# Performance work log

Hardware: AMD Instinct MI355X
Metric: run time of the kernel (lower is better)

## Reference

```python
import jax, jax.numpy as jnp
import numpy as np

Q, M, D = 4096, 65536, 1024
TOP_K = 8
EPS = 1e-12  # torch F.normalize eps default


def _l2_normalize(x, axis=-1):
    # matches torch.nn.functional.normalize(p=2): x / max(||x||, eps)
    norm = jnp.sqrt(jnp.sum(x * x, axis=axis, keepdims=True))
    return x / jnp.maximum(norm, EPS)


def setup_inputs() -> dict:
    key = jax.random.key(0)
    kq, kk, kv = jax.random.split(key, 3)
    query_embeddings = jax.random.normal(kq, (Q, D), dtype=jnp.float32)
    keys = jax.random.normal(kk, (M, D), dtype=jnp.float32)
    values = jax.random.normal(kv, (M, D), dtype=jnp.float32)
    return {"query_embeddings": query_embeddings, "keys": keys, "values": values, "top_k": TOP_K}


def reference(query_embeddings, keys, values, top_k):
    # L2-normalize queries and memory keys
    q = _l2_normalize(query_embeddings, axis=1)          # [Q, D]
    k = _l2_normalize(keys, axis=1)                      # [M, D]
    # dense cosine-similarity matmul
    sims = jnp.einsum('qd,md->qm', q, k)                 # [Q, M]
    # top-k selection (sorted descending, like torch.topk)
    topk_vals, topk_idx = jax.lax.top_k(sims, top_k)     # [Q, k]
    # irregular gather of retrieved values
    retrieved = values[topk_idx]                         # [Q, k, D]
    return retrieved
```

## Files before the change

kernel.cpp:

```cpp
#include <hip/hip_runtime.h>
#include <hip/hip_bf16.h>
#include <hip/hip_fp16.h>
#include <math.h>

#define Q_N 4096
#define M_N 65536
#define D_N 1024
#define TOPK 8
#define SEGS 32
#define KPS (M_N / SEGS)
#define CANDS (SEGS * TOPK)
#define NRES 16

#define GBM 256
#define GBN 256
#define GBK32 32
#define GNT32 (D_N / GBK32)
#define CHUNKQ 1024
#define NCHUNK (Q_N / CHUNKQ)
#define NTILES (M_N / GBM)
#define CAP 512

#define BM 128
#define BN 128
#define BK 32
#define NSUB (KPS / BN)
#define NKT (D_N / BK)
#define NSTEP (NSUB * NKT)
#define QT128 (Q_N / BM)

typedef short s16x8 __attribute__((ext_vector_type(8)));
typedef float f32x4 __attribute__((ext_vector_type(4)));

__device__ __forceinline__ bool better(float v0, int i0, float v1, int i1) {
  return (v0 > v1) || (v0 == v1 && i0 < i1);
}

__device__ __forceinline__ unsigned short f2bf(float f) {
  union { __hip_bfloat16 h; unsigned short u; } c;
  c.h = __float2bfloat16(f);
  return c.u;
}
__device__ __forceinline__ unsigned short f2h(float f) {
  union { __half h; unsigned short u; } c;
  c.h = __float2half(f);
  return c.u;
}
__device__ __forceinline__ float h2f(unsigned short u) {
  union { __half h; unsigned short u; } c;
  c.u = u;
  return __half2float(c.h);
}

__device__ __forceinline__ void gll16(void* lds, const void* g) {
  __builtin_amdgcn_global_load_lds(
      (const __attribute__((address_space(1))) unsigned int*)(uintptr_t)g,
      (__attribute__((address_space(3))) unsigned int*)(uintptr_t)lds, 16, 0, 0);
}

__global__ __launch_bounds__(256) void knorm_scale_kernel(const float* __restrict__ keys,
                                                          unsigned short* __restrict__ kb,
                                                          float* __restrict__ rnk) {
  int row = blockIdx.x;
  int tid = threadIdx.x;
  float4 v = reinterpret_cast<const float4*>(keys + (size_t)row * D_N)[tid];
  float s = v.x * v.x + v.y * v.y + v.z * v.z + v.w * v.w;
#pragma unroll
  for (int off = 32; off > 0; off >>= 1) s += __shfl_down(s, off);
  __shared__ float part[4];
  __shared__ float rs;
  int lane = tid & 63, wid = tid >> 6;
  if (lane == 0) part[wid] = s;
  __syncthreads();
  if (tid == 0) {
    float t = part[0] + part[1] + part[2] + part[3];
    rs = 1.0f / fmaxf(sqrtf(t), 1e-12f);
  }
  __syncthreads();
  float r = rs;
  ushort4 o;
  o.x = f2bf(v.x * r); o.y = f2bf(v.y * r); o.z = f2bf(v.z * r); o.w = f2bf(v.w * r);
  reinterpret_cast<ushort4*>(kb + (size_t)row * D_N)[tid] = o;
  if (tid == 0) rnk[row] = r;
}

__global__ __launch_bounds__(256) void qnorm_dual_kernel(const float* __restrict__ q,
                                                         float* __restrict__ qn,
                                                         unsigned short* __restrict__ qb) {
  int row = blockIdx.x;
  int tid = threadIdx.x;
  float4 v = reinterpret_cast<const float4*>(q + (size_t)row * D_N)[tid];
  float s = v.x * v.x + v.y * v.y + v.z * v.z + v.w * v.w;
#pragma unroll
  for (int off = 32; off > 0; off >>= 1) s += __shfl_down(s, off);
  __shared__ float part[4];
  __shared__ float rs;
  int lane = tid & 63, wid = tid >> 6;
  if (lane == 0) part[wid] = s;
  __syncthreads();
  if (tid == 0) {
    float t = part[0] + part[1] + part[2] + part[3];
    rs = 1.0f / fmaxf(sqrtf(t), 1e-12f);
  }
  __syncthreads();
  float r = rs;
  float4 o;
  o.x = v.x * r; o.y = v.y * r; o.z = v.z * r; o.w = v.w * r;
  reinterpret_cast<float4*>(qn + (size_t)row * D_N)[tid] = o;
  ushort4 ob;
  ob.x = f2bf(o.x); ob.y = f2bf(o.y); ob.z = f2bf(o.z); ob.w = f2bf(o.w);
  reinterpret_cast<ushort4*>(qb + (size_t)row * D_N)[tid] = ob;
}

__global__ __launch_bounds__(512, 2) void gemm_kernel(const unsigned short* __restrict__ qb,
                                                      const unsigned short* __restrict__ kb,
                                                      unsigned short* __restrict__ sims,
                                                      float* __restrict__ qmax,
                                                      int qchunk) {
  __shared__ __align__(16) union GSmem {
    struct {
      unsigned short A[3][GBN * GBK32];
      unsigned short B[3][GBM * GBK32];
    } ab;
    unsigned short S[GBN][GBM + 8];
  } smem;

  const int tid = threadIdx.x;
  const int lane = tid & 63;
  const int wid = tid >> 6;
  const int wq = wid & 3;
  const int wk = wid >> 2;

  const int bid = blockIdx.x;
  const int x = bid & 7;
  const int idx = bid >> 3;
  const int keyTile = (x << 5) + (idx >> 2);
  const int qTile = idx & 3;
  const int kbase = keyTile * GBM;
  const int qbase = qchunk * CHUNKQ + qTile * GBN;
  const int qloc0 = qTile * GBN;

  const int srow16 = lane >> 2;
  const int swz32 = (((lane & 3) ^ ((lane >> 2) & 3)) << 3);
  const unsigned short* aRow = qb + (size_t)(qbase + (wid << 5) + srow16) * D_N + swz32;
  const unsigned short* bRow = kb + (size_t)(kbase + (wid << 5) + srow16) * D_N + swz32;

  const int fr = lane & 15;
  const int g = lane >> 4;
  const int cp = ((g ^ (fr & 3)) << 3);

  f32x4 acc[8][4];
#pragma unroll
  for (int m = 0; m < 8; ++m)
#pragma unroll
    for (int n = 0; n < 4; ++n) acc[m][n] = (f32x4)0.0f;

#define STG_A(TT, SL)                                                         \
  {                                                                           \
    unsigned short* d = &smem.ab.A[SL][0] + (wid << 10);                      \
    const unsigned short* s = aRow + ((TT) << 5);                             \
    gll16(d, s);                                                              \
    gll16(d + 512, s + (size_t)16 * D_N);                                     \
  }
#define STG_B(TT, SL)                                                         \
  {                                                                           \
    unsigned short* d = &smem.ab.B[SL][0] + (wid << 10);                      \
    const unsigned short* s = bRow + ((TT) << 5);                             \
    gll16(d, s);                                                              \
    gll16(d + 512, s + (size_t)16 * D_N);                                     \
  }

  STG_A(0, 0) STG_B(0, 0)
  STG_A(1, 1) STG_B(1, 1)

  int slot = 0;
#pragma unroll 1
  for (int t = 0; t < GNT32; ++t) {
    if (t < GNT32 - 1) {
      asm volatile("s_waitcnt vmcnt(4)" ::: "memory");
    } else {
      asm volatile("s_waitcnt vmcnt(0)" ::: "memory");
    }
    __builtin_amdgcn_sched_barrier(0);
    __builtin_amdgcn_s_barrier();
    __builtin_amdgcn_sched_barrier(0);

    const unsigned short* Ac = &smem.ab.A[slot][0];
    const unsigned short* Bc = &smem.ab.B[slot][0];
    int nslot = slot + 2; if (nslot >= 3) nslot -= 3;
    const bool dost = (t + 2) < GNT32;

    s16x8 bq[4], af[4];

#pragma unroll
    for (int mf = 0; mf < 4; ++mf)
      af[mf] = *(const s16x8*)(Bc + ((wk << 7) + (mf << 4) + fr) * GBK32 + cp);
#pragma unroll
    for (int n = 0; n < 4; ++n)
      bq[n] = *(const s16x8*)(Ac + ((wq << 6) + (n << 4) + fr) * GBK32 + cp);
    if (dost) STG_A(t + 2, nslot)
    __builtin_amdgcn_s_barrier();
    __builtin_amdgcn_sched_barrier(0);
    asm volatile("s_waitcnt lgkmcnt(0)" ::: "memory");
    __builtin_amdgcn_sched_barrier(0);
    __builtin_amdgcn_s_setprio(1);
#pragma unroll
    for (int mf = 0; mf < 4; ++mf)
#pragma unroll
      for (int n = 0; n < 4; ++n)
        acc[mf][n] = __builtin_amdgcn_mfma_f32_16x16x32_bf16(af[mf], bq[n], acc[mf][n], 0, 0, 0);
    __builtin_amdgcn_s_setprio(0);
    __builtin_amdgcn_s_barrier();
    __builtin_amdgcn_sched_barrier(0);

#pragma unroll
    for (int mf = 0; mf < 4; ++mf)
      af[mf] = *(const s16x8*)(Bc + ((wk << 7) + 64 + (mf << 4) + fr) * GBK32 + cp);
    if (dost) STG_B(t + 2, nslot)
    __builtin_amdgcn_s_barrier();
    __builtin_amdgcn_sched_barrier(0);
    asm volatile("s_waitcnt lgkmcnt(0)" ::: "memory");
    __builtin_amdgcn_sched_barrier(0);
    __builtin_amdgcn_s_setprio(1);
#pragma unroll
    for (int mf = 0; mf < 4; ++mf)
#pragma unroll
      for (int n = 0; n < 4; ++n)
        acc[4 + mf][n] = __builtin_amdgcn_mfma_f32_16x16x32_bf16(af[mf], bq[n], acc[4 + mf][n], 0, 0, 0);
    __builtin_amdgcn_s_setprio(0);
    __builtin_amdgcn_s_barrier();
    __builtin_amdgcn_sched_barrier(0);

    ++slot; if (slot == 3) slot = 0;
  }
#undef STG_A
#undef STG_B

  __syncthreads();
#pragma unroll
  for (int m = 0; m < 8; ++m)
#pragma unroll
    for (int n = 0; n < 4; ++n)
#pragma unroll
      for (int j = 0; j < 4; ++j)
        smem.S[(wq << 6) + (n << 4) + fr][(wk << 7) + (m << 4) + (g << 2) + j] =
            f2h(acc[m][n][j]);
  __syncthreads();
#pragma unroll 1
  for (int it = 0; it < 16; ++it) {
    int cid = it * 512 + tid;
    int row = cid >> 5;
    int col = (cid & 31) << 3;
    s16x8 vv = *(const s16x8*)&smem.S[row][col];
    *(s16x8*)(sims + (size_t)(qloc0 + row) * M_N + kbase + col) = vv;
  }
  if (tid < 256) {
    float mx = -1e38f;
#pragma unroll 1
    for (int k8 = 0; k8 < 32; ++k8) {
      s16x8 vv = *(const s16x8*)&smem.S[tid][k8 << 3];
#pragma unroll
      for (int e = 0; e < 8; ++e) mx = fmaxf(mx, h2f((unsigned short)vv[e]));
    }
    qmax[(size_t)(qloc0 + tid) * NTILES + keyTile] = mx;
  }
}

__global__ __launch_bounds__(256) void scan2_kernel(const unsigned short* __restrict__ sims,
                                                    const float* __restrict__ qmax,
                                                    int* __restrict__ cand_idx,
                                                    int qchunk) {
  __shared__ float bufv[4][CAP];
  __shared__ int bufi[4][CAP];
  __shared__ int tlist[4][NTILES];
  __shared__ int cnts[4];
  __shared__ int tcnts[4];

  const int tid = threadIdx.x;
  const int lane = tid & 63;
  const int wv = tid >> 6;
  const int q = blockIdx.x * 4 + wv;
  const int qg = qchunk * CHUNKQ + q;
  const unsigned short* row = sims + (size_t)q * M_N;

  if (lane == 0) { cnts[wv] = 0; tcnts[wv] = 0; }
  __syncthreads();

  float4 m4 = *reinterpret_cast<const float4*>(qmax + (size_t)q * NTILES + (lane << 2));
  float tv[4] = {m4.x, m4.y, m4.z, m4.w};
  float keep[4] = {m4.x, m4.y, m4.z, m4.w};
  float T = -1e38f;
#pragma unroll 1
  for (int j = 0; j < 16; ++j) {
    float bv = tv[0]; int bi = (lane << 2);
#pragma unroll
    for (int s = 1; s < 4; ++s)
      if (better(tv[s], (lane << 2) + s, bv, bi)) { bv = tv[s]; bi = (lane << 2) + s; }
#pragma unroll
    for (int off = 32; off > 0; off >>= 1) {
      float ov = __shfl_xor(bv, off);
      int oi = __shfl_xor(bi, off);
      if (better(ov, oi, bv, bi)) { bv = ov; bi = oi; }
    }
    T = bv;
#pragma unroll
    for (int s = 0; s < 4; ++s)
      if ((lane << 2) + s == bi) tv[s] = -1e38f;
  }

#pragma unroll
  for (int s = 0; s < 4; ++s) {
    if (keep[s] >= T) {
      int p = atomicAdd(&tcnts[wv], 1);
      tlist[wv][p] = (lane << 2) + s;
    }
  }
  int tc = tcnts[wv];

#pragma unroll 1
  for (int i = 0; i < tc; ++i) {
    int t = tlist[wv][i];
    ushort4 pk = *reinterpret_cast<const ushort4*>(row + t * GBM + (lane << 2));
    unsigned short pe[4] = {pk.x, pk.y, pk.z, pk.w};
#pragma unroll
    for (int e = 0; e < 4; ++e) {
      float v = h2f(pe[e]);
      if (v >= T) {
        int p = atomicAdd(&cnts[wv], 1);
        if (p < CAP) { bufv[wv][p] = v; bufi[wv][p] = t * GBM + (lane << 2) + e; }
      }
    }
  }
  int n = cnts[wv];
  if (n > CAP) n = CAP;

  float cv[CAP / 64];
  int ci[CAP / 64];
#pragma unroll
  for (int s = 0; s < CAP / 64; ++s) {
    int id = s * 64 + lane;
    bool ok = id < n;
    cv[s] = ok ? bufv[wv][id] : -1e38f;
    ci[s] = ok ? bufi[wv][id] : 0;
  }
#pragma unroll 1
  for (int j = 0; j < 16; ++j) {
    float bv = cv[0]; int bi = ci[0];
#pragma unroll
    for (int s = 1; s < CAP / 64; ++s)
      if (better(cv[s], ci[s], bv, bi)) { bv = cv[s]; bi = ci[s]; }
#pragma unroll
    for (int off = 32; off > 0; off >>= 1) {
      float ov = __shfl_xor(bv, off);
      int oi = __shfl_xor(bi, off);
      if (better(ov, oi, bv, bi)) { bv = ov; bi = oi; }
    }
    if (lane == 0) cand_idx[(size_t)qg * 16 + j] = bi;
#pragma unroll
    for (int s = 0; s < CAP / 64; ++s)
      if (ci[s] == bi) cv[s] = -1e38f;
  }
}

__global__ __launch_bounds__(256) void rescore_kernel(const float* __restrict__ qn,
                                                      const float* __restrict__ keys,
                                                      const float* __restrict__ values,
                                                      const float* __restrict__ rnk,
                                                      const int* __restrict__ cand_idx,
                                                      float* __restrict__ out) {
  const int q = blockIdx.x;
  const int tid = threadIdx.x;
  const int lane = tid & 63;
  const int w = tid >> 6;
  __shared__ int si[16];
  __shared__ float rsc[16];
  if (tid < 16) si[tid] = cand_idx[(size_t)q * 16 + tid];
  __syncthreads();
  const float* qrow = &qn[(size_t)q * D_N + lane * 16];
  float4 qv0 = *reinterpret_cast<const float4*>(qrow + 0);
  float4 qv1 = *reinterpret_cast<const float4*>(qrow + 4);
  float4 qv2 = *reinterpret_cast<const float4*>(qrow + 8);
  float4 qv3 = *reinterpret_cast<const float4*>(qrow + 12);
  for (int c = w; c < 16; c += 4) {
    int id = si[c];
    const float* kr = &keys[(size_t)id * D_N + lane * 16];
    float4 k0 = *reinterpret_cast<const float4*>(kr + 0);
    float4 k1 = *reinterpret_cast<const float4*>(kr + 4);
    float4 k2 = *reinterpret_cast<const float4*>(kr + 8);
    float4 k3 = *reinterpret_cast<const float4*>(kr + 12);
    float s = qv0.x * k0.x + qv0.y * k0.y + qv0.z * k0.z + qv0.w * k0.w
            + qv1.x * k1.x + qv1.y * k1.y + qv1.z * k1.z + qv1.w * k1.w
            + qv2.x * k2.x + qv2.y * k2.y + qv2.z * k2.z + qv2.w * k2.w
            + qv3.x * k3.x + qv3.y * k3.y + qv3.z * k3.z + qv3.w * k3.w;
#pragma unroll
    for (int off = 32; off > 0; off >>= 1) s += __shfl_down(s, off);
    if (lane == 0) rsc[c] = s * rnk[id];
  }
  __syncthreads();
  __shared__ int sel[TOPK];
  if (tid == 0) {
    unsigned used = 0;
    for (int j = 0; j < TOPK; ++j) {
      int best = -1;
      for (int c = 0; c < 16; ++c) {
        if ((used >> c) & 1u) continue;
        if (best < 0 || better(rsc[c], si[c], rsc[best], si[best])) best = c;
      }
      used |= 1u << best;
      sel[j] = si[best];
    }
  }
  __syncthreads();
#pragma unroll
  for (int j = 0; j < TOPK; ++j) {
    int rowi = sel[j];
    float4 v = *reinterpret_cast<const float4*>(&values[(size_t)rowi * D_N + tid * 4]);
    *reinterpret_cast<float4*>(&out[(size_t)q * (TOPK * D_N) + j * D_N + tid * 4]) = v;
  }
}

__global__ __launch_bounds__(256, 3) void simsb_kernel(const unsigned short* __restrict__ qb,
                                                       const unsigned short* __restrict__ kb,
                                                       float* __restrict__ cand_val,
                                                       int* __restrict__ cand_idx) {
  __shared__ __align__(16) union SmemU {
    struct {
      unsigned short A[3][BM * BK];
      unsigned short B[3][BN * BK];
    } ab;
    struct {
      float v[BM * 4 * TOPK];
      int i[BM * 4 * TOPK];
    } mg;
  } smem;

  const int tid = threadIdx.x;
  const int lane = tid & 63;
  const int wid = tid >> 6;

  const int orig = blockIdx.x;
  const int x = orig & 7;
  const int idx = orig >> 3;
  const int qtile = ((x >> 1) << 3) + (idx & 7);
  const int seg = ((x & 1) << 4) + (idx >> 3);
  const int qbase = qtile * BM;
  const int segBase = seg * KPS;

  const int srow = (wid << 5) + (lane >> 2);
  const int scol = (((lane & 3) ^ ((lane >> 3) & 3)) << 3);
  const unsigned short* aSeg = qb + (size_t)(qbase + srow) * D_N + scol;
  const unsigned short* bSeg = kb + (size_t)(segBase + srow) * D_N + scol;

  const int fr = lane & 15;
  const int g = lane >> 4;
  const int chunk_phys = g ^ ((fr >> 1) & 3);
  const unsigned short* rB = &smem.ab.B[0][0] + (fr << 5) + (chunk_phys << 3);
  const unsigned short* rA = &smem.ab.A[0][0] + (((wid << 5) + fr) << 5) + (chunk_phys << 3);

  float lv[2][TOPK];
  int li[2][TOPK];
#pragma unroll
  for (int n = 0; n < 2; ++n)
#pragma unroll
    for (int j = 0; j < TOPK; ++j) { lv[n][j] = -1e30f; li[n][j] = 0x7fffffff; }

  f32x4 acc[8][2];
#pragma unroll
  for (int m = 0; m < 8; ++m)
#pragma unroll
    for (int n = 0; n < 2; ++n) acc[m][n] = (f32x4)0.0f;

#pragma unroll
  for (int p = 0; p < 2; ++p) {
    const unsigned short* aS = aSeg + (p << 5);
    const unsigned short* bS = bSeg + (p << 5);
    unsigned short* Ad = &smem.ab.A[p][0] + (wid << 10);
    unsigned short* Bd = &smem.ab.B[p][0] + (wid << 10);
    gll16(Ad, aS);
    gll16(Ad + 512, aS + (size_t)16 * D_N);
    gll16(Bd, bS);
    gll16(Bd + 512, bS + (size_t)16 * D_N);
  }

  const unsigned short* aP0 = aSeg + 64;
  const unsigned short* aP1 = aP0 + (size_t)16 * D_N;
  const unsigned short* bP0 = bSeg + 64;
  const unsigned short* bP1 = bP0 + (size_t)16 * D_N;

#define SWAIT_(N) asm volatile("s_waitcnt vmcnt(" #N ")" ::: "memory")
#define SWAIT(N) SWAIT_(N)

#define FOLD(V)                                                               \
  {                                                                           \
    const int kb0 = segBase + (((V) >> 5) << 7) + (g << 2);                   \
    _Pragma("unroll")                                                         \
    for (int n = 0; n < 2; ++n)                                               \
      _Pragma("unroll")                                                       \
      for (int m = 0; m < 8; ++m) {                                           \
        float q0 = acc[m][n][0], q1 = acc[m][n][1];                           \
        float q2 = acc[m][n][2], q3 = acc[m][n][3];                           \
        acc[m][n] = (f32x4)0.0f;                                              \
        float mx = fmaxf(fmaxf(q0, q1), fmaxf(q2, q3));                       \
        const int id0 = kb0 + (m << 4);                                       \
        if (better(mx, id0, lv[n][TOPK - 1], li[n][TOPK - 1])) {              \
          float vals[4] = {q0, q1, q2, q3};                                   \
          _Pragma("unroll")                                                   \
          for (int j = 0; j < 4; ++j) {                                       \
            float val = vals[j];                                              \
            int id = id0 + j;                                                 \
            if (better(val, id, lv[n][TOPK - 1], li[n][TOPK - 1])) {          \
              float cv = val; int ci = id;                                    \
              _Pragma("unroll")                                               \
              for (int p = 0; p < TOPK; ++p) {                                \
                if (better(cv, ci, lv[n][p], li[n][p])) {                     \
                  float tv = lv[n][p]; int ti = li[n][p];                     \
                  lv[n][p] = cv; li[n][p] = ci;                               \
                  cv = tv; ci = ti;                                           \
                }                                                             \
              }                                                               \
            }                                                                 \
          }                                                                   \
        }                                                                     \
      }                                                                       \
  }

#define STEP(V, SLOT, WAITN, RESTAGE)                                         \
  {                                                                           \
    SWAIT(WAITN);                                                             \
    __builtin_amdgcn_sched_barrier(0);                                        \
    __builtin_amdgcn_s_barrier();                                             \
    __builtin_amdgcn_sched_barrier(0);                                        \
    if (RESTAGE) {                                                            \
      unsigned short* Ad = &smem.ab.A[((SLOT) + 2) % 3][0] + (wid << 10);     \
      unsigned short* Bd = &smem.ab.B[((SLOT) + 2) % 3][0] + (wid << 10);     \
      gll16(Ad, aP0);                                                         \
      gll16(Ad + 512, aP1);                                                   \
      gll16(Bd, bP0);                                                         \
      gll16(Bd + 512, bP1);                                                   \
    }                                                                         \
    {                                                                         \
      const bool wrp = (((V) & 31) == 29);                                    \
      const int dA = wrp ? -992 : 32;                                         \
      const int dB = wrp ? 130080 : 32;                                       \
      aP0 += dA; aP1 += dA; bP0 += dB; bP1 += dB;                             \
    }                                                                         \
    s16x8 af[8], bq[2];                                                       \
    _Pragma("unroll")                                                         \
    for (int m = 0; m < 8; ++m)                                               \
      af[m] = *(const s16x8*)(rB + (SLOT) * 4096 + (m << 9));                 \
    bq[0] = *(const s16x8*)(rA + (SLOT) * 4096);                              \
    bq[1] = *(const s16x8*)(rA + (SLOT) * 4096 + 512);                        \
    __builtin_amdgcn_s_setprio(1);                                            \
    _Pragma("unroll")                                                         \
    for (int m = 0; m < 8; ++m) {                                             \
      acc[m][0] = __builtin_amdgcn_mfma_f32_16x16x32_bf16(af[m], bq[0], acc[m][0], 0, 0, 0); \
      acc[m][1] = __builtin_amdgcn_mfma_f32_16x16x32_bf16(af[m], bq[1], acc[m][1], 0, 0, 0); \
    }                                                                         \
    __builtin_amdgcn_s_setprio(0);                                            \
    if (((V) & 31) == 31) FOLD(V)                                             \
  }

#pragma unroll 1
  for (int vb = 0; vb < NSTEP - 2; vb += 3) {
    STEP(vb + 0, 0, 4, 1)
    STEP(vb + 1, 1, 4, 1)
    STEP(vb + 2, 2, 4, 1)
  }
  STEP(510, 0, 4, 0)
  STEP(511, 1, 0, 0)
#undef STEP
#undef FOLD
#undef SWAIT
#undef SWAIT_

  __syncthreads();

#pragma unroll
  for (int n = 0; n < 2; ++n) {
    const int ql = (wid << 5) + (n << 4) + fr;
#pragma unroll
    for (int j = 0; j < TOPK; ++j) {
      smem.mg.v[((ql << 2) + g) * TOPK + j] = lv[n][j];
      smem.mg.i[((ql << 2) + g) * TOPK + j] = li[n][j];
    }
  }
  __syncthreads();

  if (tid < BM) {
    const int rb = tid << 5;
    int p0 = 0, p1 = 0, p2 = 0, p3 = 0;
    size_t base = (size_t)(qbase + tid) * CANDS + seg * TOPK;
#pragma unroll
    for (int j = 0; j < TOPK; ++j) {
      float v0 = smem.mg.v[rb + 0 + p0];  int i0 = smem.mg.i[rb + 0 + p0];
      float v1 = smem.mg.v[rb + 8 + p1];  int i1 = smem.mg.i[rb + 8 + p1];
      float v2 = smem.mg.v[rb + 16 + p2]; int i2 = smem.mg.i[rb + 16 + p2];
      float v3 = smem.mg.v[rb + 24 + p3]; int i3 = smem.mg.i[rb + 24 + p3];
      float bv = v0; int bi = i0; int sel = 0;
      if (better(v1, i1, bv, bi)) { bv = v1; bi = i1; sel = 1; }
      if (better(v2, i2, bv, bi)) { bv = v2; bi = i2; sel = 2; }
      if (better(v3, i3, bv, bi)) { bv = v3; bi = i3; sel = 3; }
      cand_val[base + j] = bv;
      cand_idx[base + j] = bi;
      p0 += (sel == 0); p1 += (sel == 1); p2 += (sel == 2); p3 += (sel == 3);
    }
  }
}

__global__ __launch_bounds__(256) void merge_kernel(const float* __restrict__ qn,
                                                    const float* __restrict__ keys,
                                                    const float* __restrict__ values,
                                                    const float* __restrict__ rnk,
                                                    const float* __restrict__ cand_val,
                                                    const int* __restrict__ cand_idx,
                                                    float* __restrict__ out) {
  const int q = blockIdx.x;
  const int tid = threadIdx.x;
  const int lane = tid & 63;
  const int w = tid >> 6;
  __shared__ float sv[CANDS];
  __shared__ int si[CANDS];
  sv[tid] = cand_val[(size_t)q * CANDS + tid];
  si[tid] = cand_idx[(size_t)q * CANDS + tid];
  __syncthreads();
  for (int k = 2; k <= CANDS; k <<= 1) {
    for (int j = k >> 1; j > 0; j >>= 1) {
      int ixj = tid ^ j;
      if (ixj > tid) {
        float v0 = sv[tid], v1 = sv[ixj];
        int i0 = si[tid], i1 = si[ixj];
        bool desc = ((tid & k) == 0);
        bool dosw = desc ? better(v1, i1, v0, i0) : better(v0, i0, v1, i1);
        if (dosw) { sv[tid] = v1; si[tid] = i1; sv[ixj] = v0; si[ixj] = i0; }
      }
      __syncthreads();
    }
  }
  __shared__ float rsc[NRES];
  const float* qrow = &qn[(size_t)q * D_N + lane * 16];
  float4 qv0 = *reinterpret_cast<const float4*>(qrow + 0);
  float4 qv1 = *reinterpret_cast<const float4*>(qrow + 4);
  float4 qv2 = *reinterpret_cast<const float4*>(qrow + 8);
  float4 qv3 = *reinterpret_cast<const float4*>(qrow + 12);
  for (int c = w; c < NRES; c += 4) {
    int id = si[c];
    const float* kr = &keys[(size_t)id * D_N + lane * 16];
    float4 k0 = *reinterpret_cast<const float4*>(kr + 0);
    float4 k1 = *reinterpret_cast<const float4*>(kr + 4);
    float4 k2 = *reinterpret_cast<const float4*>(kr + 8);
    float4 k3 = *reinterpret_cast<const float4*>(kr + 12);
    float s = qv0.x * k0.x + qv0.y * k0.y + qv0.z * k0.z + qv0.w * k0.w
            + qv1.x * k1.x + qv1.y * k1.y + qv1.z * k1.z + qv1.w * k1.w
            + qv2.x * k2.x + qv2.y * k2.y + qv2.z * k2.z + qv2.w * k2.w
            + qv3.x * k3.x + qv3.y * k3.y + qv3.z * k3.z + qv3.w * k3.w;
#pragma unroll
    for (int off = 32; off > 0; off >>= 1) s += __shfl_down(s, off);
    if (lane == 0) rsc[c] = s * rnk[id];
  }
  __syncthreads();
  __shared__ int sel[TOPK];
  if (tid == 0) {
    unsigned used = 0;
    for (int j = 0; j < TOPK; ++j) {
      int best = -1;
      for (int c = 0; c < NRES; ++c) {
        if ((used >> c) & 1u) continue;
        if (best < 0 || better(rsc[c], si[c], rsc[best], si[best])) best = c;
      }
      used |= 1u << best;
      sel[j] = si[best];
    }
  }
  __syncthreads();
#pragma unroll
  for (int j = 0; j < TOPK; ++j) {
    int row = sel[j];
    float4 v = *reinterpret_cast<const float4*>(&values[(size_t)row * D_N + tid * 4]);
    *reinterpret_cast<float4*>(&out[(size_t)q * (TOPK * D_N) + j * D_N + tid * 4]) = v;
  }
}

extern "C" void kernel_launch(void* const* d_in, const int* in_sizes, int n_in,
                              void* d_out, int out_size, void* d_ws, size_t ws_size,
                              hipStream_t stream) {
  const float* query  = (const float*)d_in[0];
  const float* keys   = (const float*)d_in[1];
  const float* values = (const float*)d_in[2];
  float* out = (float*)d_out;
  char* ws = (char*)d_ws;

  const size_t offQn   = 0;
  const size_t offQb   = offQn + (size_t)Q_N * D_N * 4;
  const size_t offKb   = offQb + (size_t)Q_N * D_N * 2;
  const size_t offRnk  = offKb + (size_t)M_N * D_N * 2;
  const size_t offCv   = offRnk + (size_t)M_N * 4;
  const size_t offCi   = offCv + (size_t)Q_N * CANDS * 4;
  const size_t offSims = offCi + (size_t)Q_N * CANDS * 4;
  const size_t offQmax = offSims + (size_t)CHUNKQ * M_N * 2;
  const size_t needPrimary = offQmax + (size_t)CHUNKQ * NTILES * 4;

  float* qn = (float*)(ws + offQn);
  unsigned short* qb = (unsigned short*)(ws + offQb);
  unsigned short* kb = (unsigned short*)(ws + offKb);
  float* rnk = (float*)(ws + offRnk);
  float* cand_val = (float*)(ws + offCv);
  int* cand_idx = (int*)(ws + offCi);
  unsigned short* sims = (unsigned short*)(ws + offSims);
  float* qmax = (float*)(ws + offQmax);

  hipLaunchKernelGGL(knorm_scale_kernel, dim3(M_N), dim3(256), 0, stream, keys, kb, rnk);
  hipLaunchKernelGGL(qnorm_dual_kernel, dim3(Q_N), dim3(256), 0, stream, query, qn, qb);

  if (ws_size >= needPrimary) {
    for (int c = 0; c < NCHUNK; ++c) {
      hipLaunchKernelGGL(gemm_kernel, dim3(256 * 4), dim3(512), 0, stream,
                         qb, kb, sims, qmax, c);
      hipLaunchKernelGGL(scan2_kernel, dim3(CHUNKQ / 4), dim3(256), 0, stream,
                         sims, qmax, cand_idx, c);
    }
    hipLaunchKernelGGL(rescore_kernel, dim3(Q_N), dim3(256), 0, stream,
                       qn, keys, values, rnk, cand_idx, out);
  } else {
    hipLaunchKernelGGL(simsb_kernel, dim3(QT128 * SEGS), dim3(256), 0, stream,
                       qb, kb, cand_val, cand_idx);
    hipLaunchKernelGGL(merge_kernel, dim3(Q_N), dim3(256), 0, stream,
                       qn, keys, values, rnk, cand_val, cand_idx, out);
  }
}
```

Baseline: 893.0 us.

## Simplify GEMM main loop to single barrier and change LDS swizzle

Restructures the bf16 similarity GEMM inner loop. The old version split each k-step into two halves with separate staging and several barriers; the new one issues all global-to-LDS loads for step t+2 up front, loads all eight A fragments, and runs the 32 MFMAs with only the top-of-loop barrier. The LDS XOR swizzle also changes, on both the store side and the fragment-read side, to reduce bank conflicts. The intent is to cut barrier and waitcnt overhead. The cost is higher register pressure from holding eight fragments, and less interleaving of LDS reads with MFMA, left to the compiler scheduler.

```diff
diff --git a/kernel.cpp b/kernel.cpp
--- a/kernel.cpp
+++ b/kernel.cpp
@@ -140,14 +140,14 @@
   const int qbase = qchunk * CHUNKQ + qTile * GBN;
   const int qloc0 = qTile * GBN;
 
-  const int srow16 = lane >> 2;
-  const int swz32 = (((lane & 3) ^ ((lane >> 2) & 3)) << 3);
-  const unsigned short* aRow = qb + (size_t)(qbase + (wid << 5) + srow16) * D_N + swz32;
-  const unsigned short* bRow = kb + (size_t)(kbase + (wid << 5) + srow16) * D_N + swz32;
+  const int srow = (wid << 5) + (lane >> 2);
+  const int scol = (((lane & 3) ^ ((lane >> 3) & 3)) << 3);
+  const unsigned short* aRow = qb + (size_t)(qbase + srow) * D_N + scol;
+  const unsigned short* bRow = kb + (size_t)(kbase + srow) * D_N + scol;
 
   const int fr = lane & 15;
   const int g = lane >> 4;
-  const int cp = ((g ^ (fr & 3)) << 3);
+  const int cp = ((g ^ ((fr >> 1) & 3)) << 3);
 
   f32x4 acc[8][4];
 #pragma unroll
@@ -155,23 +155,20 @@
 #pragma unroll
     for (int n = 0; n < 4; ++n) acc[m][n] = (f32x4)0.0f;
 
-#define STG_A(TT, SL)                                                         \
+#define STG(TT, SL)                                                           \
   {                                                                           \
-    unsigned short* d = &smem.ab.A[SL][0] + (wid << 10);                      \
-    const unsigned short* s = aRow + ((TT) << 5);                             \
-    gll16(d, s);                                                              \
-    gll16(d + 512, s + (size_t)16 * D_N);                                     \
-  }
-#define STG_B(TT, SL)                                                         \
-  {                                                                           \
-    unsigned short* d = &smem.ab.B[SL][0] + (wid << 10);                      \
-    const unsigned short* s = bRow + ((TT) << 5);                             \
-    gll16(d, s);                                                              \
-    gll16(d + 512, s + (size_t)16 * D_N);                                     \
-  }
-
-  STG_A(0, 0) STG_B(0, 0)
-  STG_A(1, 1) STG_B(1, 1)
+    unsigned short* Ad = &smem.ab.A[SL][0] + (wid << 10);                     \
+    unsigned short* Bd = &smem.ab.B[SL][0] + (wid << 10);                     \
+    const unsigned short* as_ = aRow + ((TT) << 5);                           \
+    const unsigned short* bs_ = bRow + ((TT) << 5);                           \
+    gll16(Ad, as_);                                                           \
+    gll16(Bd, bs_);                                                           \
+    gll16(Ad + 512, as_ + (size_t)16 * D_N);                                  \
+    gll16(Bd + 512, bs_ + (size_t)16 * D_N);                                  \
+  }
+
+  STG(0, 0)
+  STG(1, 1)
 
   int slot = 0;
 #pragma unroll 1
@@ -188,53 +185,27 @@
     const unsigned short* Ac = &smem.ab.A[slot][0];
     const unsigned short* Bc = &smem.ab.B[slot][0];
     int nslot = slot + 2; if (nslot >= 3) nslot -= 3;
-    const bool dost = (t + 2) < GNT32;
-
-    s16x8 bq[4], af[4];
-
-#pragma unroll
-    for (int mf = 0; mf < 4; ++mf)
-      af[mf] = *(const s16x8*)(Bc + ((wk << 7) + (mf << 4) + fr) * GBK32 + cp);
+    if (t + 2 < GNT32) STG(t + 2, nslot)
+
+    s16x8 bq[4], af[8];
 #pragma unroll
     for (int n = 0; n < 4; ++n)
       bq[n] = *(const s16x8*)(Ac + ((wq << 6) + (n << 4) + fr) * GBK32 + cp);
-    if (dost) STG_A(t + 2, nslot)
-    __builtin_amdgcn_s_barrier();
-    __builtin_amdgcn_sched_barrier(0);
-    asm volatile("s_waitcnt lgkmcnt(0)" ::: "memory");
-    __builtin_amdgcn_sched_barrier(0);
+#pragma unroll
+    for (int m = 0; m < 8; ++m)
+      af[m] = *(const s16x8*)(Bc + ((wk << 7) + (m << 4) + fr) * GBK32 + cp);
+
     __builtin_amdgcn_s_setprio(1);
 #pragma unroll
-    for (int mf = 0; mf < 4; ++mf)
+    for (int m = 0; m < 8; ++m)
 #pragma unroll
       for (int n = 0; n < 4; ++n)
-        acc[mf][n] = __builtin_amdgcn_mfma_f32_16x16x32_bf16(af[mf], bq[n], acc[mf][n], 0, 0, 0);
+        acc[m][n] = __builtin_amdgcn_mfma_f32_16x16x32_bf16(af[m], bq[n], acc[m][n], 0, 0, 0);
     __builtin_amdgcn_s_setprio(0);
-    __builtin_amdgcn_s_barrier();
-    __builtin_amdgcn_sched_barrier(0);
-
-#pragma unroll
-    for (int mf = 0; mf < 4; ++mf)
-      af[mf] = *(const s16x8*)(Bc + ((wk << 7) + 64 + (mf << 4) + fr) * GBK32 + cp);
-    if (dost) STG_B(t + 2, nslot)
-    __builtin_amdgcn_s_barrier();
-    __builtin_amdgcn_sched_barrier(0);
-    asm volatile("s_waitcnt lgkmcnt(0)" ::: "memory");
-    __builtin_amdgcn_sched_barrier(0);
-    __builtin_amdgcn_s_setprio(1);
-#pragma unroll
-    for (int mf = 0; mf < 4; ++mf)
-#pragma unroll
-      for (int n = 0; n < 4; ++n)
-        acc[4 + mf][n] = __builtin_amdgcn_mfma_f32_16x16x32_bf16(af[mf], bq[n], acc[4 + mf][n], 0, 0, 0);
-    __builtin_amdgcn_s_setprio(0);
-    __builtin_amdgcn_s_barrier();
-    __builtin_amdgcn_sched_barrier(0);
 
     ++slot; if (slot == 3) slot = 0;
   }
-#undef STG_A
-#undef STG_B
+#undef STG
 
   __syncthreads();
 #pragma unroll
```

New measurement: 874.8 us. -2.0%, faster.
